# Optimization experiments

Measured on AMD Instinct MI355X. Metric: run time of the kernel, lower is better.

Reference implementation:

```python
import jax, jax.numpy as jnp
import numpy as np

B, L, C = 2, 2048, 1024
H = 16
HD = C // H  # head_features = 64


def setup_inputs() -> dict:
    key = jax.random.key(0)
    k1, k2, k3, k4, k5, k6 = jax.random.split(key, 6)
    input_x = jax.random.normal(k1, (B, L, C), dtype=jnp.float32)
    x_mask = jax.random.randint(k2, (B, 1, 1, L), 0, 2, dtype=jnp.int32)
    s = 1.0 / np.sqrt(C)
    W_qkv = jax.random.normal(k3, (C, 3 * C), dtype=jnp.float32) * s
    b_qkv = jax.random.normal(k4, (3 * C,), dtype=jnp.float32) * 0.01
    W_proj = jax.random.normal(k5, (C, C), dtype=jnp.float32) * s
    b_proj = jax.random.normal(k6, (C,), dtype=jnp.float32) * 0.01
    return {"input_x": input_x, "x_mask": x_mask, "W_qkv": W_qkv,
            "b_qkv": b_qkv, "W_proj": W_proj, "b_proj": b_proj}


def reference(input_x, x_mask, W_qkv, b_qkv, W_proj, b_proj):
    # qkv projection: [B,L,3C] -> [3,B,H,L,HD]
    qkv = input_x @ W_qkv + b_qkv
    qkv = qkv.reshape(B, L, 3, H, HD).transpose(2, 0, 3, 1, 4)
    q, k, v = qkv[0], qkv[1], qkv[2]
    q = q * (HD ** -0.5)  # first scale (module applies it to q)
    scores = jnp.einsum('bhld,bhmd->bhlm', q, k)  # [B,H,L,L]
    scores = jnp.where(x_mask == 1, jnp.float32(-1e10), scores)
    scores = scores / jnp.sqrt(jnp.float32(HD))  # module's second scale (faithful quirk)
    probs = jax.nn.softmax(scores, axis=-1)
    out = jnp.einsum('bhlm,bhmd->bhld', probs, v)  # [B,H,L,HD]
    out = out.transpose(0, 2, 1, 3).reshape(B, L, C)
    return out @ W_proj + b_proj
```

## Files before the change

### kernel.cpp

```cpp
#include <hip/hip_runtime.h>
#include <stdint.h>

typedef __attribute__((ext_vector_type(8))) short short8;
typedef __attribute__((ext_vector_type(4))) short short4v;
typedef __attribute__((ext_vector_type(4))) float floatx4;
typedef __attribute__((ext_vector_type(16))) float floatx16;

#define B_ 2
#define L_ 2048
#define C_ 1024
#define H_ 16
#define HD_ 64

#define QSCALE (0.015625f * 1.44269504088896f)
#define MASKVAL (-1.8033688e9f)

__device__ __forceinline__ unsigned short f2bf(float f) {
  union { float f; uint32_t u; } v; v.f = f;
  uint32_t r = 0x7FFFu + ((v.u >> 16) & 1u);
  return (unsigned short)((v.u + r) >> 16);
}

__device__ __forceinline__ uint32_t cvtpk(float lo, float hi) {
  uint32_t r;
  asm("v_cvt_pk_bf16_f32 %0, %1, %2" : "=v"(r) : "v"(lo), "v"(hi));
  return r;
}

__device__ __forceinline__ unsigned short f2bf_hw(float f) {
  return (unsigned short)cvtpk(f, f);
}

__device__ __forceinline__ void pl32swap(uint32_t& a, uint32_t& b) {
  asm volatile("v_permlane32_swap_b32 %0, %1" : "+v"(a), "+v"(b));
}

__device__ __forceinline__ void async16(const void* g, void* l) {
  __builtin_amdgcn_global_load_lds(
      (const __attribute__((address_space(1))) void*)g,
      (__attribute__((address_space(3))) void*)l, 16, 0, 0);
}

__global__ __launch_bounds__(256) void prep_k(const float* __restrict__ x,
                                              unsigned short* __restrict__ Xb,
                                              const int* __restrict__ mask,
                                              unsigned short* __restrict__ maskbf) {
  int bid = blockIdx.x;
  if (bid < 2048) {
    int i = (bid * 256 + threadIdx.x) * 8;
    floatx4 a = *(const floatx4*)(x + i);
    floatx4 b = *(const floatx4*)(x + i + 4);
    short8 o;
    o[0] = (short)f2bf(a[0]); o[1] = (short)f2bf(a[1]);
    o[2] = (short)f2bf(a[2]); o[3] = (short)f2bf(a[3]);
    o[4] = (short)f2bf(b[0]); o[5] = (short)f2bf(b[1]);
    o[6] = (short)f2bf(b[2]); o[7] = (short)f2bf(b[3]);
    *(short8*)(Xb + i) = o;
  } else if (maskbf) {
    int i = (bid - 2048) * 256 + threadIdx.x;
    if (i < B_ * L_) maskbf[i] = (mask[i] == 1) ? f2bf(MASKVAL) : (unsigned short)0;
  }
}

__global__ __launch_bounds__(256) void maskpre_k(const int* __restrict__ mask,
                                                 unsigned short* __restrict__ maskbf) {
  int i = blockIdx.x * 256 + threadIdx.x;
  if (i < B_ * L_) maskbf[i] = (mask[i] == 1) ? f2bf(MASKVAL) : (unsigned short)0;
}

__global__ __launch_bounds__(256) void transpose2_k(const float* __restrict__ W1,
                                                    unsigned short* __restrict__ O1,
                                                    const float* __restrict__ W2,
                                                    unsigned short* __restrict__ O2) {
  const int z = blockIdx.z;
  if (z == 1 && blockIdx.x >= C_ / 32) return;
  const float* in = z ? W2 : W1;
  unsigned short* out = z ? O2 : O1;
  const int Cc = z ? C_ : 3 * C_;
  __shared__ float tile[32][33];
  int tx = threadIdx.x, ty = threadIdx.y;
  int c0 = blockIdx.x * 32, r0 = blockIdx.y * 32;
#pragma unroll
  for (int i = 0; i < 4; i++)
    tile[ty + i * 8][tx] = in[(r0 + ty + i * 8) * Cc + c0 + tx];
  __syncthreads();
#pragma unroll
  for (int i = 0; i < 4; i++)
    out[(c0 + ty + i * 8) * C_ + r0 + tx] = f2bf(tile[tx][ty + i * 8]);
}

template <int EPI, int BN>
__global__ __launch_bounds__(256) void gemm128(const unsigned short* __restrict__ A,
                                               const unsigned short* __restrict__ BT, int K,
                                               int nbx,
                                               const float* __restrict__ bias,
                                               unsigned short* __restrict__ outQ,
                                               unsigned short* __restrict__ outK,
                                               unsigned short* __restrict__ outVT,
                                               float* __restrict__ outF) {
  __shared__ __attribute__((aligned(16))) unsigned short Asmem[2][128 * 32];
  __shared__ __attribute__((aligned(16))) unsigned short Bsmem[2][BN * 32];
  const int t = threadIdx.x;
  const int wave = t >> 6, lane = t & 63;
  const int wr = wave >> 1, wc = wave & 1;
  const int NW = BN / 2;
  const int NF = BN / 32;
  const int nwg = gridDim.x;
  const int id = (blockIdx.x & 7) * (nwg >> 3) + (blockIdx.x >> 3);
  const int bx = id % nbx, by = id / nbx;
  const int row0 = by * 128, col0 = bx * BN;

  const int arow = row0 + (t >> 2), brow = col0 + (t >> 2);
  const int koff = (t & 3) * 8;

#define STAGE(buf, k0)                                                                 \
  {                                                                                    \
    async16(A + (size_t)arow * K + (k0) + koff, &Asmem[buf][t * 8]);                   \
    async16(A + (size_t)(arow + 64) * K + (k0) + koff, &Asmem[buf][(256 + t) * 8]);    \
    async16(BT + (size_t)brow * K + (k0) + koff, &Bsmem[buf][t * 8]);                  \
    if (BN == 128)                                                                     \
      async16(BT + (size_t)(brow + 64) * K + (k0) + koff, &Bsmem[buf][(256 + t) * 8]); \
  }

  floatx4 acc[4][NF] = {};
  STAGE(0, 0);
  __syncthreads();
  int cur = 0;
  for (int k0 = 0; k0 < K; k0 += 32) {
    if (k0 + 32 < K) STAGE(cur ^ 1, k0 + 32);
    short8 af[4], bfr[NF];
#pragma unroll
    for (int m = 0; m < 4; m++)
      af[m] = *(const short8*)(&Asmem[cur][(wr * 64 + m * 16 + (lane & 15)) * 32 +
                                           (lane >> 4) * 8]);
#pragma unroll
    for (int n = 0; n < NF; n++)
      bfr[n] = *(const short8*)(&Bsmem[cur][(wc * NW + n * 16 + (lane & 15)) * 32 +
                                            (lane >> 4) * 8]);
#pragma unroll
    for (int m = 0; m < 4; m++)
#pragma unroll
      for (int n = 0; n < NF; n++)
        acc[m][n] = __builtin_amdgcn_mfma_f32_16x16x32_bf16(af[m], bfr[n], acc[m][n], 0, 0, 0);
    __syncthreads();
    cur ^= 1;
  }
#undef STAGE

#pragma unroll
  for (int m = 0; m < 4; m++)
#pragma unroll
    for (int n = 0; n < NF; n++) {
      const int r0e = row0 + wr * 64 + m * 16 + (lane >> 4) * 4;
      const int cc = col0 + wc * NW + n * 16 + (lane & 15);
      const float bv = bias[cc];
      if (EPI == 2) {
#pragma unroll
        for (int j = 0; j < 4; j++)
          outF[(size_t)(r0e + j) * C_ + cc] = acc[m][n][j] + bv;
      } else {
        const int which = col0 >> 10;
        const int rem = cc & 1023, h = rem >> 6, d = rem & 63;
        const int bb = r0e >> 11, l0 = r0e & 2047;
        const size_t base = (size_t)(bb * H_ + h) * (L_ * HD_);
        if (which == 0) {
#pragma unroll
          for (int j = 0; j < 4; j++)
            outQ[base + (size_t)(l0 + j) * HD_ + d] = f2bf_hw((acc[m][n][j] + bv) * QSCALE);
        } else if (which == 1) {
          const size_t kbase =
              base + ((l0 >> 5) * 8 + (d >> 4) * 2 + ((d >> 3) & 1)) * 256 + (d & 7);
#pragma unroll
          for (int j = 0; j < 4; j++)
            outK[kbase + ((l0 & 31) + j) * 8] = f2bf_hw(acc[m][n][j] + bv);
        } else {
          const size_t vbase = base +
                               ((((l0 >> 7) * 2 + (d >> 5)) * 8 + ((l0 >> 4) & 7)) * 2 +
                                ((l0 >> 3) & 1)) * 256 +
                               (d & 31) * 8 + (l0 & 7);
          union { unsigned short s[4]; short4v v; } ov;
#pragma unroll
          for (int j = 0; j < 4; j++) ov.s[j] = f2bf_hw(acc[m][n][j] + bv);
          *(short4v*)(outVT + vbase) = ov.v;
        }
      }
    }
}

__global__ __launch_bounds__(256) void attn_k(const unsigned short* __restrict__ Q,
                                              const unsigned short* __restrict__ Kf,
                                              const unsigned short* __restrict__ VTf,
                                              const unsigned short* __restrict__ maskbf,
                                              unsigned short* __restrict__ attn_out) {
  __shared__ __attribute__((aligned(16))) unsigned short Ks[128 * 64];
  __shared__ __attribute__((aligned(16))) unsigned short VTs[64 * 128];
  __shared__ __attribute__((aligned(16))) unsigned short maskLb[L_];

  const int t = threadIdx.x, wave = t >> 6, lane = t & 63;
  const int h = lane >> 5, c32 = lane & 31;
  const int bh = blockIdx.x & 31;
  const int qt = blockIdx.x >> 5;
  const int b = bh >> 4, hh = bh & 15;
  const unsigned short* Qp = Q + (size_t)bh * L_ * HD_;
  const unsigned short* Kp = Kf + (size_t)bh * L_ * HD_;
  const unsigned short* VTp = VTf + (size_t)bh * L_ * HD_;
  const int qrow = qt * 128 + wave * 32 + c32;

  short8 qf[4];
#pragma unroll
  for (int ks = 0; ks < 4; ks++)
    qf[ks] = *(const short8*)(Qp + (size_t)qrow * HD_ + ks * 16 + h * 8);

  union { uint32_t u[4]; short8 v; } onef;
  onef.u[0] = h ? 0u : 0x3F80u;
  onef.u[1] = 0; onef.u[2] = 0; onef.u[3] = 0;
  floatx16 z16;
#pragma unroll
  for (int e = 0; e < 16; e++) z16[e] = 0.f;

  async16(maskbf + b * L_ + t * 8, maskLb + t * 8);

  floatx16 o[2] = {};
  float lrun = 0.f;

  for (int kv = 0; kv < 16; kv++) {
    __syncthreads();
#pragma unroll
    for (int i = 0; i < 4; i++) {
      int idx = i * 256 + t;
      async16(Kp + (size_t)kv * 8192 + idx * 8, Ks + idx * 8);
    }
#pragma unroll
    for (int i = 0; i < 4; i++) {
      int idx = i * 256 + t;
      async16(VTp + (size_t)kv * 8192 + idx * 8, VTs + idx * 8);
    }
    __syncthreads();

    floatx16 s[4];
#pragma unroll
    for (int kg = 0; kg < 4; kg++) {
      union { uint32_t u[4]; short8 v; } mf;
      unsigned short mval = maskLb[kv * 128 + kg * 32 + c32];
      mf.u[0] = h ? 0u : (uint32_t)mval;
      mf.u[1] = 0; mf.u[2] = 0; mf.u[3] = 0;
      s[kg] = __builtin_amdgcn_mfma_f32_32x32x16_bf16(mf.v, onef.v, z16, 0, 0, 0);
#pragma unroll
      for (int ks = 0; ks < 4; ks++) {
        const short8 kfr = *(const short8*)(Ks + ((kg * 4 + ks) * 2 + h) * 256 + c32 * 8);
        s[kg] = __builtin_amdgcn_mfma_f32_32x32x16_bf16(kfr, qf[ks], s[kg], 0, 0, 0);
      }
    }

    float r0 = 0.f, r1 = 0.f, r2 = 0.f, r3 = 0.f;
#pragma unroll
    for (int kg = 0; kg < 4; kg++)
#pragma unroll
      for (int q = 0; q < 4; q++) {
        float p0 = __builtin_amdgcn_exp2f(s[kg][4 * q + 0]);
        float p1 = __builtin_amdgcn_exp2f(s[kg][4 * q + 1]);
        float p2 = __builtin_amdgcn_exp2f(s[kg][4 * q + 2]);
        float p3 = __builtin_amdgcn_exp2f(s[kg][4 * q + 3]);
        s[kg][4 * q + 0] = p0; s[kg][4 * q + 1] = p1;
        s[kg][4 * q + 2] = p2; s[kg][4 * q + 3] = p3;
        r0 += p0; r1 += p1; r2 += p2; r3 += p3;
      }
    float rs = (r0 + r1) + (r2 + r3);
    rs += __shfl_xor(rs, 32);
    lrun += rs;

#pragma unroll
    for (int kg = 0; kg < 4; kg++) {
      uint32_t pk[8];
#pragma unroll
      for (int e = 0; e < 8; e++) pk[e] = cvtpk(s[kg][2 * e], s[kg][2 * e + 1]);
#pragma unroll
      for (int ts = 0; ts < 2; ts++) {
        uint32_t x0 = pk[4 * ts + 0], x1 = pk[4 * ts + 1];
        uint32_t y0 = pk[4 * ts + 2], y1 = pk[4 * ts + 3];
        pl32swap(x0, y0);
        pl32swap(x1, y1);
        union { uint32_t u[4]; short8 v; } pf;
        pf.u[0] = x0; pf.u[1] = x1; pf.u[2] = y0; pf.u[3] = y1;
        const int kt = kg * 2 + ts;
#pragma unroll
        for (int dg = 0; dg < 2; dg++) {
          const short8 vfr =
              *(const short8*)(VTs + ((dg * 8 + kt) * 2 + h) * 256 + c32 * 8);
          o[dg] = __builtin_amdgcn_mfma_f32_32x32x16_bf16(vfr, pf.v, o[dg], 0, 0, 0);
        }
      }
    }
  }

  const float inv = 1.f / lrun;
#pragma unroll
  for (int dg = 0; dg < 2; dg++)
#pragma unroll
    for (int rr = 0; rr < 4; rr++) {
      short4v ov;
#pragma unroll
      for (int jj = 0; jj < 4; jj++) ov[jj] = (short)f2bf(o[dg][rr * 4 + jj] * inv);
      int d0 = dg * 32 + rr * 8 + h * 4;
      *(short4v*)(attn_out + ((size_t)b * L_ + qrow) * C_ + hh * HD_ + d0) = ov;
    }
}

extern "C" void kernel_launch(void* const* d_in, const int* in_sizes, int n_in,
                              void* d_out, int out_size, void* d_ws, size_t ws_size,
                              hipStream_t stream) {
  const float* x = (const float*)d_in[0];
  const int* mask = (const int*)d_in[1];
  const float* Wqkv = (const float*)d_in[2];
  const float* bqkv = (const float*)d_in[3];
  const float* Wproj = (const float*)d_in[4];
  const float* bproj = (const float*)d_in[5];
  float* out = (float*)d_out;
  char* ws = (char*)d_ws;

  unsigned short* Xb = (unsigned short*)(ws);
  unsigned short* WqkvT = (unsigned short*)(ws + (8u << 20));
  unsigned short* WprojT = (unsigned short*)(ws + (14u << 20));
  unsigned short* Qb = (unsigned short*)(ws + (16u << 20));
  unsigned short* Kb = (unsigned short*)(ws + (24u << 20));
  unsigned short* VTb = (unsigned short*)(ws + (32u << 20));
  unsigned short* AOb = Xb;

  const bool fused_mask = ws_size >= ((size_t)(40u << 20) + 8192);
  unsigned short* maskbf = fused_mask ? (unsigned short*)(ws + (40u << 20))
                                      : (unsigned short*)(ws + (8u << 20));

  prep_k<<<2064, 256, 0, stream>>>(x, Xb, mask, fused_mask ? maskbf : nullptr);

  dim3 tb(32, 8);
  transpose2_k<<<dim3(3 * C_ / 32, C_ / 32, 2), tb, 0, stream>>>(Wqkv, WqkvT, Wproj, WprojT);

  gemm128<1, 128><<<768, 256, 0, stream>>>(Xb, WqkvT, C_, 24, bqkv, Qb, Kb, VTb, nullptr);

  if (!fused_mask) maskpre_k<<<(B_ * L_) / 256, 256, 0, stream>>>(mask, maskbf);

  attn_k<<<B_ * H_ * (L_ / 128), 256, 0, stream>>>(Qb, Kb, VTb, maskbf, AOb);

  gemm128<2, 64><<<512, 256, 0, stream>>>(AOb, WprojT, C_, 16, bproj, nullptr, nullptr, nullptr,
                                          out);
}
```

Before: 113.9 us.

## Split KV range across two wave groups in attention and merge partial outputs

The attention block grows from 256 to 512 threads. Each half of the block processes half of the key/value sequence for the same 128 query rows, using separate shared-memory buffers, and the two partial accumulators and row sums are combined through shared memory at the end. This doubles the waves per query tile to hide MFMA and load latency while halving the sequential KV loop. The cost is twice the LDS per block, which may lower occupancy, plus an extra reduction and sync. It relies on the softmax having no running max, so partial sums add directly.

```diff
diff --git a/kernel.cpp b/kernel.cpp
--- a/kernel.cpp
+++ b/kernel.cpp
@@ -187,24 +187,25 @@
     }
 }
 
-__global__ __launch_bounds__(256) void attn_k(const unsigned short* __restrict__ Q,
+__global__ __launch_bounds__(512) void attn_k(const unsigned short* __restrict__ Q,
                                               const unsigned short* __restrict__ Kf,
                                               const unsigned short* __restrict__ VTf,
                                               const unsigned short* __restrict__ maskbf,
                                               unsigned short* __restrict__ attn_out) {
-  __shared__ __attribute__((aligned(16))) unsigned short Ks[128 * 64];
-  __shared__ __attribute__((aligned(16))) unsigned short VTs[64 * 128];
+  __shared__ __attribute__((aligned(16))) unsigned short Ks[2 * 128 * 64];
+  __shared__ __attribute__((aligned(16))) unsigned short VTs[2 * 64 * 128];
   __shared__ __attribute__((aligned(16))) unsigned short maskLb[L_];
 
   const int t = threadIdx.x, wave = t >> 6, lane = t & 63;
   const int h = lane >> 5, c32 = lane & 31;
+  const int half = wave >> 2, wq = wave & 3;
   const int bh = blockIdx.x & 31;
   const int qt = blockIdx.x >> 5;
   const int b = bh >> 4, hh = bh & 15;
   const unsigned short* Qp = Q + (size_t)bh * L_ * HD_;
   const unsigned short* Kp = Kf + (size_t)bh * L_ * HD_;
   const unsigned short* VTp = VTf + (size_t)bh * L_ * HD_;
-  const int qrow = qt * 128 + wave * 32 + c32;
+  const int qrow = qt * 128 + wq * 32 + c32;
 
   short8 qf[4];
 #pragma unroll
@@ -218,36 +219,41 @@
 #pragma unroll
   for (int e = 0; e < 16; e++) z16[e] = 0.f;
 
-  async16(maskbf + b * L_ + t * 8, maskLb + t * 8);
+  if (t < 256) async16(maskbf + b * L_ + t * 8, maskLb + t * 8);
 
   floatx16 o[2] = {};
   float lrun = 0.f;
 
-  for (int kv = 0; kv < 16; kv++) {
+  const unsigned short* KsW = Ks + half * 8192;
+  const unsigned short* VTsW = VTs + half * 8192;
+
+  for (int step = 0; step < 8; step++) {
     __syncthreads();
 #pragma unroll
     for (int i = 0; i < 4; i++) {
-      int idx = i * 256 + t;
-      async16(Kp + (size_t)kv * 8192 + idx * 8, Ks + idx * 8);
+      int idx = i * 512 + t, hf = idx >> 10, off = idx & 1023;
+      async16(Kp + (size_t)(step + 8 * hf) * 8192 + off * 8, Ks + idx * 8);
     }
 #pragma unroll
     for (int i = 0; i < 4; i++) {
-      int idx = i * 256 + t;
-      async16(VTp + (size_t)kv * 8192 + idx * 8, VTs + idx * 8);
+      int idx = i * 512 + t, hf = idx >> 10, off = idx & 1023;
+      async16(VTp + (size_t)(step + 8 * hf) * 8192 + off * 8, VTs + idx * 8);
     }
     __syncthreads();
+
+    const int moff = (step + 8 * half) * 128;
 
     floatx16 s[4];
 #pragma unroll
     for (int kg = 0; kg < 4; kg++) {
       union { uint32_t u[4]; short8 v; } mf;
-      unsigned short mval = maskLb[kv * 128 + kg * 32 + c32];
+      unsigned short mval = maskLb[moff + kg * 32 + c32];
       mf.u[0] = h ? 0u : (uint32_t)mval;
       mf.u[1] = 0; mf.u[2] = 0; mf.u[3] = 0;
       s[kg] = __builtin_amdgcn_mfma_f32_32x32x16_bf16(mf.v, onef.v, z16, 0, 0, 0);
 #pragma unroll
       for (int ks = 0; ks < 4; ks++) {
-        const short8 kfr = *(const short8*)(Ks + ((kg * 4 + ks) * 2 + h) * 256 + c32 * 8);
+        const short8 kfr = *(const short8*)(KsW + ((kg * 4 + ks) * 2 + h) * 256 + c32 * 8);
         s[kg] = __builtin_amdgcn_mfma_f32_32x32x16_bf16(kfr, qf[ks], s[kg], 0, 0, 0);
       }
     }
@@ -286,24 +292,45 @@
 #pragma unroll
         for (int dg = 0; dg < 2; dg++) {
           const short8 vfr =
-              *(const short8*)(VTs + ((dg * 8 + kt) * 2 + h) * 256 + c32 * 8);
+              *(const short8*)(VTsW + ((dg * 8 + kt) * 2 + h) * 256 + c32 * 8);
           o[dg] = __builtin_amdgcn_mfma_f32_32x32x16_bf16(vfr, pf.v, o[dg], 0, 0, 0);
         }
       }
     }
   }
 
-  const float inv = 1.f / lrun;
-#pragma unroll
-  for (int dg = 0; dg < 2; dg++)
-#pragma unroll
-    for (int rr = 0; rr < 4; rr++) {
-      short4v ov;
-#pragma unroll
-      for (int jj = 0; jj < 4; jj++) ov[jj] = (short)f2bf(o[dg][rr * 4 + jj] * inv);
-      int d0 = dg * 32 + rr * 8 + h * 4;
-      *(short4v*)(attn_out + ((size_t)b * L_ + qrow) * C_ + hh * HD_ + d0) = ov;
-    }
+  __syncthreads();
+  float* Os = (float*)Ks;
+  float* Ls = (float*)VTs;
+  const int qlocal = wq * 32 + c32;
+  if (half == 1) {
+#pragma unroll
+    for (int dg = 0; dg < 2; dg++)
+#pragma unroll
+      for (int rr = 0; rr < 4; rr++) {
+        floatx4 q4;
+#pragma unroll
+        for (int jj = 0; jj < 4; jj++) q4[jj] = o[dg][rr * 4 + jj];
+        *(floatx4*)(Os + qlocal * 64 + dg * 32 + rr * 8 + h * 4) = q4;
+      }
+    if (h == 0) Ls[qlocal] = lrun;
+  }
+  __syncthreads();
+  if (half == 0) {
+    const float inv = 1.f / (lrun + Ls[qlocal]);
+#pragma unroll
+    for (int dg = 0; dg < 2; dg++)
+#pragma unroll
+      for (int rr = 0; rr < 4; rr++) {
+        const int d0 = dg * 32 + rr * 8 + h * 4;
+        floatx4 q4 = *(const floatx4*)(Os + qlocal * 64 + d0);
+        short4v ov;
+#pragma unroll
+        for (int jj = 0; jj < 4; jj++)
+          ov[jj] = (short)f2bf((o[dg][rr * 4 + jj] + q4[jj]) * inv);
+        *(short4v*)(attn_out + ((size_t)b * L_ + qrow) * C_ + hh * HD_ + d0) = ov;
+      }
+  }
 }
 
 extern "C" void kernel_launch(void* const* d_in, const int* in_sizes, int n_in,
@@ -339,7 +366,7 @@
 
   if (!fused_mask) maskpre_k<<<(B_ * L_) / 256, 256, 0, stream>>>(mask, maskbf);
 
-  attn_k<<<B_ * H_ * (L_ / 128), 256, 0, stream>>>(Qb, Kb, VTb, maskbf, AOb);
+  attn_k<<<B_ * H_ * (L_ / 128), 512, 0, stream>>>(Qb, Kb, VTb, maskbf, AOb);
 
   gemm128<2, 64><<<512, 256, 0, stream>>>(AOb, WprojT, C_, 16, bproj, nullptr, nullptr, nullptr,
                                           out);
```

Result: slower. 119.7 us (+5.0%).
